# Performance work log

Measured on AMD Instinct MI355X. Metric: run time of the kernel, lower is better.

Reference implementation:

```python
import jax, jax.numpy as jnp
import numpy as np

N = 100_000   # nodes
E = 1_600_000 # edges
D = 64        # in = hidden = out channels
EPS = 1e-8


def setup_inputs() -> dict:
    key = jax.random.key(0)
    ks = jax.random.split(key, 6)
    s = 1.0 / np.sqrt(D)
    return {
        "x": jax.random.normal(ks[0], (N, D), jnp.float32),
        "edge_index": jax.random.randint(ks[1], (2, E), 0, N, dtype=jnp.int32),
        "W0": jax.random.normal(ks[2], (D, D), jnp.float32) * s,
        "b0": jnp.zeros((D,), jnp.float32),
        "Wm": jax.random.normal(ks[3], (D, D), jnp.float32) * s,
        "bm": jnp.zeros((D,), jnp.float32),
        "W1": jax.random.normal(ks[4], (D, D), jnp.float32) * s,
        "b1": jnp.zeros((D,), jnp.float32),
    }


def _proj_normalize(y):
    # projective (hyperbolic) renormalization onto the unit sphere in R^D
    return y / (jnp.linalg.norm(y, axis=-1, keepdims=True) + EPS)


def _hyp_linear(x, W, b):
    return _proj_normalize(x @ W + b)


def _hinner(u, v):
    # UHG (hyperbolic) bilinear form: <u,v> = u_1..d-1 . v_1..d-1 - u_d * v_d
    return jnp.sum(u[..., :-1] * v[..., :-1], axis=-1) - u[..., -1] * v[..., -1]


def _cross_ratio(x):
    a, b, c, d = x[0], x[1], x[2], x[3]
    return (_hinner(a, c) * _hinner(b, d)) / (_hinner(a, d) * _hinner(b, c) + EPS)


def _maybe_restore_cr(x, cr_init):
    # restore_cross_ratio: rescale x so the 4-point cross-ratio matches cr_init,
    # applied only when the torch guard conditions hold (finite, non-degenerate).
    cr_cur = _cross_ratio(x[:4])
    ratio = cr_init / (cr_cur + EPS)
    cond = ((~jnp.isnan(cr_cur)) & (~jnp.isnan(cr_init))
            & (jnp.abs(cr_cur) > EPS) & (jnp.abs(cr_init) > EPS)
            & (ratio > EPS))
    scale = jnp.where(cond, jnp.sqrt(jnp.abs(ratio)), 1.0)
    x_r = x * scale
    ok = jnp.all(jnp.isfinite(x_r))
    return jnp.where(cond & ok, x_r, x)


def _message_passing(x, src, dst, Wm, bm):
    # gather -> mean-aggregate(scatter) -> hyperbolic linear, preserving cross-ratio
    cr0 = _cross_ratio(x[:4])
    msgs = x[src]                                                  # [E, D] gather
    summed = jax.ops.segment_sum(msgs, dst, num_segments=N)        # [N, D] scatter-add
    cnt = jax.ops.segment_sum(jnp.ones((E,), x.dtype), dst, num_segments=N)
    agg = summed / jnp.maximum(cnt, 1.0)[:, None]                  # mean aggregation
    h = _proj_normalize(agg @ Wm + bm)
    return _maybe_restore_cr(h, cr0)


def reference(x, edge_index, W0, b0, Wm, bm, W1, b1):
    src, dst = edge_index[0], edge_index[1]
    cr_init = _cross_ratio(x[:4])          # N > 3 so has_cr is always True
    h = _hyp_linear(x, W0, b0)             # layers[0]
    # num_layers = 2 -> single message-passing round (i = 1)
    h = _message_passing(h, src, dst, Wm, bm)
    h = _hyp_linear(h, W1, b1)             # layers[1]
    h = jax.nn.relu(h)                      # act
    h = _maybe_restore_cr(h, cr_init)
    return h
```

## Files before the change

kernel.cpp:

```cpp
#include <hip/hip_runtime.h>
#include <math.h>

#define NNODES 100000
#define NEDGES 1600000
#define DD 64
#define EPS 1e-8f

#define NBUCK 1024
#define BW 98
#define BIN_BLOCKS 256
#define BIN_CHUNK ((NEDGES + BIN_BLOCKS - 1) / BIN_BLOCKS)
#define BIN_CAP 16
#define SORT_CAP 4096
#define NTILES (NNODES / 16)
#define CAP4 512
#define TSTR 68

typedef unsigned short us8 __attribute__((ext_vector_type(8)));
typedef short short8 __attribute__((ext_vector_type(8)));
typedef float f32x4 __attribute__((ext_vector_type(4)));

__device__ __forceinline__ float wave_sum(float v) {
    #pragma unroll
    for (int off = 32; off; off >>= 1) v += __shfl_xor(v, off, 64);
    return v;
}

__device__ __forceinline__ float hinner(float u, float v, float sgn) {
    return wave_sum(sgn * u * v);
}

__device__ __forceinline__ float cross_ratio(float r0, float r1, float r2, float r3, float sgn) {
    float A = hinner(r0, r2, sgn);
    float B = hinner(r1, r3, sgn);
    float C = hinner(r0, r3, sgn);
    float Dv = hinner(r1, r2, sgn);
    return (A * B) / (C * Dv + EPS);
}

__device__ __forceinline__ float restore_scale(float cr_i, float cr_c) {
    float ratio = cr_i / (cr_c + EPS);
    bool cond = (!__builtin_isnan(cr_c)) && (!__builtin_isnan(cr_i)) &&
                (fabsf(cr_c) > EPS) && (fabsf(cr_i) > EPS) && (ratio > EPS);
    float s = 1.0f;
    if (cond) {
        s = sqrtf(fabsf(ratio));
        if (!__builtin_isfinite(s)) s = 1.0f;
    }
    return s;
}

__device__ __forceinline__ unsigned short f2bf(float f) {
    unsigned u = __float_as_uint(f);
    unsigned r = (u + 0x7fffu + ((u >> 16) & 1u)) >> 16;
    return (unsigned short)r;
}

__device__ __forceinline__ float bf2f(unsigned short b) {
    return __uint_as_float(((unsigned)b) << 16);
}

__device__ __forceinline__ float bcast(float v, int lane) {
    return __int_as_float(__builtin_amdgcn_readlane(__float_as_int(v), lane));
}

__device__ __forceinline__ void load_bfrags(const float* __restrict__ W, int lane,
                                            short8 bhi[4][2], short8 blo[4][2]) {
    int c = lane & 15, q = lane >> 4;
    #pragma unroll
    for (int t = 0; t < 4; t++)
        #pragma unroll
        for (int h = 0; h < 2; h++) {
            short8 hi8, lo8;
            #pragma unroll
            for (int j = 0; j < 8; j++) {
                float w = W[(h * 32 + q * 8 + j) * DD + t * 16 + c];
                unsigned short hb = f2bf(w);
                float r = w - bf2f(hb);
                hi8[j] = (short)hb;
                lo8[j] = (short)f2bf(r);
            }
            bhi[t][h] = hi8;
            blo[t][h] = lo8;
        }
}

__device__ __forceinline__ void build_a8(const float av[8], short8& hi, short8& lo) {
    short8 h8, l8;
    #pragma unroll
    for (int j = 0; j < 8; j++) {
        unsigned short hb = f2bf(av[j]);
        float r = av[j] - bf2f(hb);
        h8[j] = (short)hb;
        l8[j] = (short)f2bf(r);
    }
    hi = h8;
    lo = l8;
}

__device__ __forceinline__ void build_a(const float* p, short8& hi, short8& lo) {
    float4 f0 = *(const float4*)p;
    float4 f1 = *(const float4*)(p + 4);
    float av[8] = {f0.x, f0.y, f0.z, f0.w, f1.x, f1.y, f1.z, f1.w};
    build_a8(av, hi, lo);
}

#define MFMA3R(cacc, ahi, alo, BH, BL, t, h)                                     \
    cacc = __builtin_amdgcn_mfma_f32_16x16x32_bf16(ahi, BH[t][h], cacc, 0, 0, 0); \
    cacc = __builtin_amdgcn_mfma_f32_16x16x32_bf16(alo, BH[t][h], cacc, 0, 0, 0); \
    cacc = __builtin_amdgcn_mfma_f32_16x16x32_bf16(ahi, BL[t][h], cacc, 0, 0, 0);

__global__ __launch_bounds__(256, 3) void k_l0h(const float* __restrict__ x,
                                                const float* __restrict__ W0,
                                                const float* __restrict__ b0,
                                                unsigned short* __restrict__ h0b,
                                                const int* __restrict__ ei,
                                                int* __restrict__ bhist) {
    __shared__ int h[NBUCK];
    if (blockIdx.x < 512) {
        for (int i = threadIdx.x; i < NBUCK; i += 256) h[i] = 0;
        __syncthreads();
        int tid = blockIdx.x * 256 + threadIdx.x;
        int stride = 512 * 256;
        for (int e = tid; e < NEDGES; e += stride)
            atomicAdd(&h[(unsigned)ei[NEDGES + e] / BW], 1);
        __syncthreads();
        for (int i = threadIdx.x; i < NBUCK; i += 256)
            if (h[i]) atomicAdd(&bhist[i], h[i]);
        return;
    }
    int bid = blockIdx.x - 512;
    int lane = threadIdx.x & 63;
    int c = lane & 15, q = lane >> 4;
    short8 bhi[4][2], blo[4][2];
    load_bfrags(W0, lane, bhi, blo);
    float badd[4];
    #pragma unroll
    for (int t = 0; t < 4; t++) badd[t] = b0[t * 16 + c];
    int wid = (bid * 256 + threadIdx.x) >> 6;
    int nw = (1024 * 256) >> 6;
    for (int tile = wid; tile < NTILES; tile += nw) {
        int R = tile * 16;
        f32x4 cc[4] = {{0, 0, 0, 0}, {0, 0, 0, 0}, {0, 0, 0, 0}, {0, 0, 0, 0}};
        #pragma unroll
        for (int hh = 0; hh < 2; hh++) {
            short8 ahi, alo;
            build_a(x + ((size_t)(R + c) << 6) + hh * 32 + q * 8, ahi, alo);
            #pragma unroll
            for (int t = 0; t < 4; t++) { MFMA3R(cc[t], ahi, alo, bhi, blo, t, hh); }
        }
        float ss[4];
        #pragma unroll
        for (int r = 0; r < 4; r++) {
            #pragma unroll
            for (int t = 0; t < 4; t++) cc[t][r] += badd[t];
            ss[r] = cc[0][r] * cc[0][r] + cc[1][r] * cc[1][r] +
                    cc[2][r] * cc[2][r] + cc[3][r] * cc[3][r];
        }
        #pragma unroll
        for (int off = 1; off <= 8; off <<= 1) {
            #pragma unroll
            for (int r = 0; r < 4; r++) ss[r] += __shfl_xor(ss[r], off, 64);
        }
        #pragma unroll
        for (int r = 0; r < 4; r++) {
            float sc = 1.0f / (sqrtf(ss[r]) + EPS);
            int row = R + q * 4 + r;
            #pragma unroll
            for (int t = 0; t < 4; t++)
                h0b[(size_t)row * DD + t * 16 + c] = f2bf(cc[t][r] * sc);
        }
    }
}

__global__ __launch_bounds__(NBUCK) void k_scan1024(const int* __restrict__ bhist,
                                                    int* __restrict__ bstart,
                                                    int* __restrict__ gcur,
                                                    int* __restrict__ scratch_cur) {
    __shared__ int s[NBUCK];
    int t = threadIdx.x;
    int v = bhist[t];
    s[t] = v;
    __syncthreads();
    for (int off = 1; off < NBUCK; off <<= 1) {
        int u = (t >= off) ? s[t - off] : 0;
        __syncthreads();
        s[t] += u;
        __syncthreads();
    }
    bstart[t] = s[t] - v;
    gcur[t] = s[t] - v;
    if (t == 0) scratch_cur[0] = 0;
}

__global__ __launch_bounds__(256) void k_bin(const int* __restrict__ ei,
                                             int* __restrict__ gcur,
                                             unsigned* __restrict__ colpack,
                                             int* __restrict__ cnt4,
                                             int* __restrict__ list4) {
    __shared__ unsigned stag[NBUCK * BIN_CAP];
    __shared__ int lcnt[NBUCK];
    int t = threadIdx.x;
    for (int i = t; i < NBUCK; i += 256) lcnt[i] = 0;
    __syncthreads();
    int lo = blockIdx.x * BIN_CHUNK;
    int hi = lo + BIN_CHUNK; if (hi > NEDGES) hi = NEDGES;
    for (int e = lo + t; e < hi; e += 256) {
        int d = ei[NEDGES + e];
        int s = ei[e];
        if ((unsigned)d < 4u) {
            int p = atomicAdd(&cnt4[d], 1);
            if (p < CAP4) list4[d * CAP4 + p] = s;
        }
        unsigned b = (unsigned)d / BW;
        unsigned dl = (unsigned)d - b * BW;
        unsigned pk = ((unsigned)s << 8) | dl;
        int slot = atomicAdd(&lcnt[b], 1);
        if (slot < BIN_CAP) {
            stag[b * BIN_CAP + slot] = pk;
        } else {
            colpack[atomicAdd(&gcur[b], 1)] = pk;
        }
    }
    __syncthreads();
    for (int b = t; b < NBUCK; b += 256) {
        int cnt = lcnt[b];
        if (cnt > BIN_CAP) cnt = BIN_CAP;
        if (cnt > 0) {
            int base = atomicAdd(&gcur[b], cnt);
            for (int i = 0; i < cnt; i++)
                colpack[base + i] = stag[b * BIN_CAP + i];
        }
    }
}

__global__ __launch_bounds__(512, 4) void k_sortAggH(const unsigned* __restrict__ colpack,
                                                     const int* __restrict__ bstart,
                                                     const int* __restrict__ bhist,
                                                     const unsigned short* __restrict__ h0b,
                                                     float* __restrict__ agg,
                                                     int* __restrict__ scratch,
                                                     int* __restrict__ scratch_cur,
                                                     const float* __restrict__ x,
                                                     const float* __restrict__ W0,
                                                     const float* __restrict__ b0,
                                                     const int* __restrict__ cnt4,
                                                     const int* __restrict__ list4,
                                                     const float* __restrict__ Wm,
                                                     const float* __restrict__ bm,
                                                     const float* __restrict__ W1,
                                                     const float* __restrict__ b1,
                                                     float* __restrict__ scal) {
    __shared__ int lcol[SORT_CAP];
    __shared__ int cnt[BW];
    __shared__ int pre[BW];
    __shared__ int sbs;
    int t = threadIdx.x;
    if (blockIdx.x == 0) {
        float* hs  = (float*)lcol;
        float* h2s = hs + 4 * DD;
        float* frs = h2s + 4 * DD;
        int lane = t & 63;
        int w = t >> 6;
        float sgn = (lane == 63) ? -1.0f : 1.0f;
        float s1 = 1.0f;
        float cr_init = 0.0f;
        if (w < 4) {
            float w0[DD];
            #pragma unroll
            for (int k = 0; k < DD; k++) w0[k] = W0[k * DD + lane];
            float b0v = b0[lane];
            auto h0row = [&](int r) -> float {
                float xv = x[(size_t)r * DD + lane];
                float acc = b0v;
                #pragma unroll
                for (int k = 0; k < DD; k++)
                    acc = fmaf(bcast(xv, k), w0[k], acc);
                float n = sqrtf(wave_sum(acc * acc));
                return acc / (n + EPS);
            };
            hs[w * DD + lane] = h0row(w);
            int full = cnt4[w];
            int cl = full; if (cl > CAP4) cl = CAP4;
            float sum = 0.0f;
            for (int i = 0; i < cl; i++) sum += h0row(list4[w * CAP4 + i]);
            float av = sum / fmaxf((float)full, 1.0f);
            float acc = bm[lane];
            #pragma unroll
            for (int k = 0; k < DD; k++)
                acc = fmaf(bcast(av, k), Wm[k * DD + lane], acc);
            float n = sqrtf(wave_sum(acc * acc));
            h2s[w * DD + lane] = acc / (n + EPS);
        }
        __syncthreads();
        if (w < 4) {
            cr_init = cross_ratio(x[lane], x[DD + lane], x[2 * DD + lane], x[3 * DD + lane], sgn);
            float cr0 = cross_ratio(hs[lane], hs[DD + lane], hs[2 * DD + lane], hs[3 * DD + lane], sgn);
            float cr_cur = cross_ratio(h2s[lane], h2s[DD + lane], h2s[2 * DD + lane], h2s[3 * DD + lane], sgn);
            s1 = restore_scale(cr0, cr_cur);
            float hv = h2s[w * DD + lane] * s1;
            float acc2 = b1[lane];
            #pragma unroll
            for (int k = 0; k < DD; k++)
                acc2 = fmaf(bcast(hv, k), W1[k * DD + lane], acc2);
            float n = sqrtf(wave_sum(acc2 * acc2));
            frs[w * DD + lane] = fmaxf(acc2 / (n + EPS), 0.0f);
        }
        __syncthreads();
        if (w == 0) {
            float cr2 = cross_ratio(frs[lane], frs[DD + lane], frs[2 * DD + lane], frs[3 * DD + lane], sgn);
            float s2 = restore_scale(cr_init, cr2);
            if (lane == 0) { scal[0] = s1; scal[1] = s2; }
        }
        return;
    }
    int b = blockIdx.x - 1;
    int nlo = b * BW; if (nlo > NNODES) nlo = NNODES;
    int nhi = nlo + BW; if (nhi > NNODES) nhi = NNODES;
    int nodes = nhi - nlo;
    int base = bstart[b];
    int n = bhist[b];
    for (int i = t; i < BW; i += 512) cnt[i] = 0;
    bool inLds = (n <= SORT_CAP);
    if (t == 0) sbs = inLds ? 0 : atomicAdd(scratch_cur, n);
    __syncthreads();
    int sb = sbs;
    for (int i = t; i < n; i += 512)
        atomicAdd(&cnt[colpack[base + i] & 255u], 1);
    __syncthreads();
    if (t < 64) {
        int v0 = cnt[t];
        int inc0 = v0;
        #pragma unroll
        for (int off = 1; off < 64; off <<= 1) {
            int u = __shfl_up(inc0, off, 64);
            if (t >= off) inc0 += u;
        }
        int tot0 = __builtin_amdgcn_readlane(inc0, 63);
        int ex0 = inc0 - v0;
        int i1 = 64 + t;
        int v1 = (i1 < BW) ? cnt[i1] : 0;
        int inc1 = v1;
        #pragma unroll
        for (int off = 1; off < 64; off <<= 1) {
            int u = __shfl_up(inc1, off, 64);
            if (t >= off) inc1 += u;
        }
        int ex1 = inc1 - v1 + tot0;
        pre[t] = ex0;
        cnt[t] = ex0;
        if (i1 < BW) { pre[i1] = ex1; cnt[i1] = ex1; }
    }
    __syncthreads();
    for (int i = t; i < n; i += 512) {
        unsigned pk = colpack[base + i];
        int pos = atomicAdd(&cnt[pk & 255u], 1);
        int v = (int)(pk >> 8);
        if (inLds) lcol[pos] = v;
        else       scratch[sb + pos] = v;
    }
    __syncthreads();
    int wv = t >> 6, lane = t & 63;
    int q = lane & 7, g = lane >> 3;
    auto run_agg = [&](auto ld) {
        for (int dl = wv; dl < nodes; dl += 8) {
            int start = pre[dl];
            int end = cnt[dl];
            float s[8] = {0, 0, 0, 0, 0, 0, 0, 0};
            int j0 = start;
            for (; j0 + 16 <= end; j0 += 16) {
                int s0 = ld(j0 + g);
                int s1i = ld(j0 + 8 + g);
                us8 u0 = *(const us8*)(h0b + (size_t)s0 * DD + q * 8);
                us8 u1 = *(const us8*)(h0b + (size_t)s1i * DD + q * 8);
                #pragma unroll
                for (int i = 0; i < 8; i++)
                    s[i] += bf2f(u0[i]) + bf2f(u1[i]);
            }
            for (; j0 < end; j0 += 8) {
                int e = j0 + g;
                bool val = e < end;
                int src = 0;
                if (val) src = ld(e);
                us8 u = *(const us8*)(h0b + (size_t)src * DD + q * 8);
                float f = val ? 1.0f : 0.0f;
                #pragma unroll
                for (int i = 0; i < 8; i++)
                    s[i] = fmaf(f, bf2f(u[i]), s[i]);
            }
            #pragma unroll
            for (int i = 0; i < 8; i++) {
                s[i] += __shfl_xor(s[i], 8, 64);
                s[i] += __shfl_xor(s[i], 16, 64);
                s[i] += __shfl_xor(s[i], 32, 64);
            }
            if (g == 0) {
                float inv = 1.0f / fmaxf((float)(end - start), 1.0f);
                float4* dst = (float4*)(agg + (size_t)(nlo + dl) * DD + q * 8);
                float4 o0 = {s[0] * inv, s[1] * inv, s[2] * inv, s[3] * inv};
                float4 o1 = {s[4] * inv, s[5] * inv, s[6] * inv, s[7] * inv};
                dst[0] = o0;
                dst[1] = o1;
            }
        }
    };
    if (inLds) run_agg([&](int e) { return lcol[e]; });
    else       run_agg([&](int e) { return scratch[sb + e]; });
}

__global__ __launch_bounds__(256, 2) void k_gemm2(float* data,
                                                  const float* __restrict__ Wm,
                                                  const float* __restrict__ bm,
                                                  const float* __restrict__ W1,
                                                  const float* __restrict__ b1,
                                                  const float* __restrict__ scal) {
    __shared__ float tsm[4][16 * TSTR];
    int tid = threadIdx.x;
    int wv = tid >> 6, lane = tid & 63;
    int c = lane & 15, q = lane >> 4;
    short8 bhiM[4][2], bloM[4][2], bhi1[4][2], blo1[4][2];
    load_bfrags(Wm, lane, bhiM, bloM);
    load_bfrags(W1, lane, bhi1, blo1);
    float bmv[4], b1v[4];
    #pragma unroll
    for (int t = 0; t < 4; t++) { bmv[t] = bm[t * 16 + c]; b1v[t] = b1[t * 16 + c]; }
    float s1 = scal[0], s2 = scal[1];
    int wid = (blockIdx.x * 256 + tid) >> 6;
    int nw = (gridDim.x * 256) >> 6;
    for (int tile = wid; tile < NTILES; tile += nw) {
        int R = tile * 16;
        f32x4 cc[4] = {{0, 0, 0, 0}, {0, 0, 0, 0}, {0, 0, 0, 0}, {0, 0, 0, 0}};
        #pragma unroll
        for (int hh = 0; hh < 2; hh++) {
            short8 ahi, alo;
            build_a(data + ((size_t)(R + c) << 6) + hh * 32 + q * 8, ahi, alo);
            #pragma unroll
            for (int t = 0; t < 4; t++) { MFMA3R(cc[t], ahi, alo, bhiM, bloM, t, hh); }
        }
        float ss[4];
        #pragma unroll
        for (int r = 0; r < 4; r++) {
            #pragma unroll
            for (int t = 0; t < 4; t++) cc[t][r] += bmv[t];
            ss[r] = cc[0][r] * cc[0][r] + cc[1][r] * cc[1][r] +
                    cc[2][r] * cc[2][r] + cc[3][r] * cc[3][r];
        }
        #pragma unroll
        for (int off = 1; off <= 8; off <<= 1) {
            #pragma unroll
            for (int r = 0; r < 4; r++) ss[r] += __shfl_xor(ss[r], off, 64);
        }
        #pragma unroll
        for (int r = 0; r < 4; r++) {
            float sc = s1 / (sqrtf(ss[r]) + EPS);
            #pragma unroll
            for (int t = 0; t < 4; t++)
                tsm[wv][(q * 4 + r) * TSTR + t * 16 + c] = cc[t][r] * sc;
        }
        f32x4 c2[4] = {{0, 0, 0, 0}, {0, 0, 0, 0}, {0, 0, 0, 0}, {0, 0, 0, 0}};
        #pragma unroll
        for (int hh = 0; hh < 2; hh++) {
            const float* p = &tsm[wv][c * TSTR + hh * 32 + q * 8];
            float av[8];
            #pragma unroll
            for (int j = 0; j < 8; j++) av[j] = p[j];
            short8 ahi, alo;
            build_a8(av, ahi, alo);
            #pragma unroll
            for (int t = 0; t < 4; t++) { MFMA3R(c2[t], ahi, alo, bhi1, blo1, t, hh); }
        }
        #pragma unroll
        for (int r = 0; r < 4; r++) {
            #pragma unroll
            for (int t = 0; t < 4; t++) c2[t][r] += b1v[t];
            ss[r] = c2[0][r] * c2[0][r] + c2[1][r] * c2[1][r] +
                    c2[2][r] * c2[2][r] + c2[3][r] * c2[3][r];
        }
        #pragma unroll
        for (int off = 1; off <= 8; off <<= 1) {
            #pragma unroll
            for (int r = 0; r < 4; r++) ss[r] += __shfl_xor(ss[r], off, 64);
        }
        #pragma unroll
        for (int r = 0; r < 4; r++) {
            float sc = 1.0f / (sqrtf(ss[r]) + EPS);
            int row = R + q * 4 + r;
            #pragma unroll
            for (int t = 0; t < 4; t++)
                data[(size_t)row * DD + t * 16 + c] = fmaxf(c2[t][r] * sc, 0.0f) * s2;
        }
    }
}

extern "C" void kernel_launch(void* const* d_in, const int* in_sizes, int n_in,
                              void* d_out, int out_size, void* d_ws, size_t ws_size,
                              hipStream_t stream) {
    const float* x  = (const float*)d_in[0];
    const int*   ei = (const int*)d_in[1];
    const float* W0 = (const float*)d_in[2];
    const float* b0 = (const float*)d_in[3];
    const float* Wm = (const float*)d_in[4];
    const float* bm = (const float*)d_in[5];
    const float* W1 = (const float*)d_in[6];
    const float* b1 = (const float*)d_in[7];
    float* out = (float*)d_out;

    unsigned short* h0b = (unsigned short*)d_ws;
    int* scratch = (int*)(h0b + (size_t)NNODES * DD);
    unsigned* colpack = (unsigned*)(scratch + NNODES);
    int* bhist  = (int*)(colpack + NEDGES);
    int* cnt4   = bhist + NBUCK;
    int* bstart = cnt4 + 4;
    int* gcur   = bstart + NBUCK;
    int* scur   = gcur + NBUCK;
    int* list4  = scur + 1;
    float* scal = (float*)(list4 + 4 * CAP4);

    (void)hipMemsetAsync(bhist, 0, (NBUCK + 4) * sizeof(int), stream);

    k_l0h     <<<1536, 256, 0, stream>>>(x, W0, b0, h0b, ei, bhist);
    k_scan1024<<<1, NBUCK, 0, stream>>>(bhist, bstart, gcur, scur);
    k_bin     <<<BIN_BLOCKS, 256, 0, stream>>>(ei, gcur, colpack, cnt4, list4);
    k_sortAggH<<<NBUCK, 512, 0, stream>>>(colpack, bstart, bhist, h0b, out, scratch, scur,
                                          x, W0, b0, cnt4, list4, Wm, bm, W1, b1, scal);
    k_gemm2   <<<512, 256, 0, stream>>>(out, Wm, bm, W1, b1, scal);
}
```

Before: 215.7 us.

## Assign one node per 8-lane group in aggregation instead of one node per wave

The gather/mean-aggregation loop now gives each 8-lane group its own destination node, so a wave handles 8 nodes at once rather than splitting one node's edges across its 8 groups. This removes the three cross-group shuffle reductions per node, and each group walks its node's edges four at a time with predicated loads. Iterations are padded to the largest degree among the wave's 8 nodes, which adds masked work for imbalanced degrees. The launch-bounds occupancy hint is also raised from 4 to 6, which may limit registers per thread.

```diff
diff --git a/kernel.cpp b/kernel.cpp
--- a/kernel.cpp
+++ b/kernel.cpp
@@ -234,7 +234,7 @@
     }
 }
 
-__global__ __launch_bounds__(512, 4) void k_sortAggH(const unsigned* __restrict__ colpack,
+__global__ __launch_bounds__(512, 6) void k_sortAggH(const unsigned* __restrict__ colpack,
                                                      const int* __restrict__ bstart,
                                                      const int* __restrict__ bhist,
                                                      const unsigned short* __restrict__ h0b,
@@ -362,40 +362,53 @@
     __syncthreads();
     int wv = t >> 6, lane = t & 63;
     int q = lane & 7, g = lane >> 3;
+    int S = wv * 8 + g;
     auto run_agg = [&](auto ld) {
-        for (int dl = wv; dl < nodes; dl += 8) {
-            int start = pre[dl];
-            int end = cnt[dl];
+        for (int b0 = 0; b0 < nodes; b0 += 64) {
+            int dl = b0 + S;
+            bool nv = dl < nodes;
+            int start = nv ? pre[dl] : 0;
+            int end   = nv ? cnt[dl] : 0;
+            int deg = end - start;
+            int md = deg, m1;
+            m1 = __shfl_xor(md, 8, 64);  md = md > m1 ? md : m1;
+            m1 = __shfl_xor(md, 16, 64); md = md > m1 ? md : m1;
+            m1 = __shfl_xor(md, 32, 64); md = md > m1 ? md : m1;
             float s[8] = {0, 0, 0, 0, 0, 0, 0, 0};
-            int j0 = start;
-            for (; j0 + 16 <= end; j0 += 16) {
-                int s0 = ld(j0 + g);
-                int s1i = ld(j0 + 8 + g);
+            int j = 0;
+            for (; j + 4 <= md; j += 4) {
+                int e0 = (j + 0 < deg) ? start + j + 0 : 0;
+                int e1 = (j + 1 < deg) ? start + j + 1 : 0;
+                int e2 = (j + 2 < deg) ? start + j + 2 : 0;
+                int e3 = (j + 3 < deg) ? start + j + 3 : 0;
+                int s0 = ld(e0), s1i = ld(e1), s2i = ld(e2), s3i = ld(e3);
+                us8 u0 = *(const us8*)(h0b + (size_t)s0  * DD + q * 8);
+                us8 u1 = *(const us8*)(h0b + (size_t)s1i * DD + q * 8);
+                us8 u2 = *(const us8*)(h0b + (size_t)s2i * DD + q * 8);
+                us8 u3 = *(const us8*)(h0b + (size_t)s3i * DD + q * 8);
+                float f0 = (j + 0 < deg) ? 1.0f : 0.0f;
+                float f1 = (j + 1 < deg) ? 1.0f : 0.0f;
+                float f2 = (j + 2 < deg) ? 1.0f : 0.0f;
+                float f3 = (j + 3 < deg) ? 1.0f : 0.0f;
+                #pragma unroll
+                for (int i = 0; i < 8; i++) {
+                    s[i] = fmaf(f0, bf2f(u0[i]), s[i]);
+                    s[i] = fmaf(f1, bf2f(u1[i]), s[i]);
+                    s[i] = fmaf(f2, bf2f(u2[i]), s[i]);
+                    s[i] = fmaf(f3, bf2f(u3[i]), s[i]);
+                }
+            }
+            for (; j < md; j++) {
+                int e0 = (j < deg) ? start + j : 0;
+                int s0 = ld(e0);
                 us8 u0 = *(const us8*)(h0b + (size_t)s0 * DD + q * 8);
-                us8 u1 = *(const us8*)(h0b + (size_t)s1i * DD + q * 8);
+                float f0 = (j < deg) ? 1.0f : 0.0f;
                 #pragma unroll
                 for (int i = 0; i < 8; i++)
-                    s[i] += bf2f(u0[i]) + bf2f(u1[i]);
+                    s[i] = fmaf(f0, bf2f(u0[i]), s[i]);
             }
-            for (; j0 < end; j0 += 8) {
-                int e = j0 + g;
-                bool val = e < end;
-                int src = 0;
-                if (val) src = ld(e);
-                us8 u = *(const us8*)(h0b + (size_t)src * DD + q * 8);
-                float f = val ? 1.0f : 0.0f;
-                #pragma unroll
-                for (int i = 0; i < 8; i++)
-                    s[i] = fmaf(f, bf2f(u[i]), s[i]);
-            }
-            #pragma unroll
-            for (int i = 0; i < 8; i++) {
-                s[i] += __shfl_xor(s[i], 8, 64);
-                s[i] += __shfl_xor(s[i], 16, 64);
-                s[i] += __shfl_xor(s[i], 32, 64);
-            }
-            if (g == 0) {
-                float inv = 1.0f / fmaxf((float)(end - start), 1.0f);
+            if (nv) {
+                float inv = 1.0f / fmaxf((float)deg, 1.0f);
                 float4* dst = (float4*)(agg + (size_t)(nlo + dl) * DD + q * 8);
                 float4 o0 = {s[0] * inv, s[1] * inv, s[2] * inv, s[3] * inv};
                 float4 o1 = {s[4] * inv, s[5] * inv, s[6] * inv, s[7] * inv};
```

After: 223.3 us. 3.5% more time.

## Fold bucket scan into histogram kernel and precompute per-node degrees

Applied to the files above, without the earlier changes.

The histogram blocks of the first kernel now also count per-node in-degree with global atomics. The last histogram block to finish, found through an atomic counter, runs the 1024-bucket exclusive scan, so the separate scan kernel launch goes away. The sort/aggregate kernel seeds its per-node counts from the precomputed degrees, skipping its LDS-atomic counting pass over colpack. In exchange it adds 1.6M random global atomics and an extra 400KB memset. The degree array aliases the overflow scratch buffer, which could be corrupted if any bucket spills out of LDS.

```diff
diff --git a/kernel.cpp b/kernel.cpp
--- a/kernel.cpp
+++ b/kernel.cpp
@@ -115,18 +115,60 @@
                                                 const float* __restrict__ b0,
                                                 unsigned short* __restrict__ h0b,
                                                 const int* __restrict__ ei,
-                                                int* __restrict__ bhist) {
+                                                int* __restrict__ bhist,
+                                                int* __restrict__ deg,
+                                                int* __restrict__ lbctr,
+                                                int* __restrict__ bstart,
+                                                int* __restrict__ gcur,
+                                                int* __restrict__ scur) {
     __shared__ int h[NBUCK];
+    __shared__ int wtot[4];
+    __shared__ int lastf;
     if (blockIdx.x < 512) {
         for (int i = threadIdx.x; i < NBUCK; i += 256) h[i] = 0;
         __syncthreads();
         int tid = blockIdx.x * 256 + threadIdx.x;
         int stride = 512 * 256;
-        for (int e = tid; e < NEDGES; e += stride)
-            atomicAdd(&h[(unsigned)ei[NEDGES + e] / BW], 1);
+        for (int e = tid; e < NEDGES; e += stride) {
+            int d = ei[NEDGES + e];
+            atomicAdd(&h[(unsigned)d / BW], 1);
+            atomicAdd(&deg[d], 1);
+        }
         __syncthreads();
         for (int i = threadIdx.x; i < NBUCK; i += 256)
             if (h[i]) atomicAdd(&bhist[i], h[i]);
+        __threadfence();
+        if (threadIdx.x == 0) lastf = (atomicAdd(lbctr, 1) == 511);
+        __syncthreads();
+        if (!lastf) return;
+        __threadfence();
+        int t = threadIdx.x;
+        int v[4];
+        int s = 0;
+        #pragma unroll
+        for (int k = 0; k < 4; k++) {
+            v[k] = atomicAdd(&bhist[t * 4 + k], 0);
+            s += v[k];
+        }
+        int lane = t & 63, w = t >> 6;
+        int inc = s;
+        #pragma unroll
+        for (int off = 1; off < 64; off <<= 1) {
+            int u = __shfl_up(inc, off, 64);
+            if (lane >= off) inc += u;
+        }
+        if (lane == 63) wtot[w] = inc;
+        __syncthreads();
+        int wbase = 0;
+        for (int i = 0; i < w; i++) wbase += wtot[i];
+        int run = wbase + inc - s;
+        #pragma unroll
+        for (int k = 0; k < 4; k++) {
+            bstart[t * 4 + k] = run;
+            gcur[t * 4 + k] = run;
+            run += v[k];
+        }
+        if (t == 0) scur[0] = 0;
         return;
     }
     int bid = blockIdx.x - 512;
@@ -171,26 +213,6 @@
                 h0b[(size_t)row * DD + t * 16 + c] = f2bf(cc[t][r] * sc);
         }
     }
-}
-
-__global__ __launch_bounds__(NBUCK) void k_scan1024(const int* __restrict__ bhist,
-                                                    int* __restrict__ bstart,
-                                                    int* __restrict__ gcur,
-                                                    int* __restrict__ scratch_cur) {
-    __shared__ int s[NBUCK];
-    int t = threadIdx.x;
-    int v = bhist[t];
-    s[t] = v;
-    __syncthreads();
-    for (int off = 1; off < NBUCK; off <<= 1) {
-        int u = (t >= off) ? s[t - off] : 0;
-        __syncthreads();
-        s[t] += u;
-        __syncthreads();
-    }
-    bstart[t] = s[t] - v;
-    gcur[t] = s[t] - v;
-    if (t == 0) scratch_cur[0] = 0;
 }
 
 __global__ __launch_bounds__(256) void k_bin(const int* __restrict__ ei,
@@ -237,6 +259,7 @@
 __global__ __launch_bounds__(512, 4) void k_sortAggH(const unsigned* __restrict__ colpack,
                                                      const int* __restrict__ bstart,
                                                      const int* __restrict__ bhist,
+                                                     const int* __restrict__ deg,
                                                      const unsigned short* __restrict__ h0b,
                                                      float* __restrict__ agg,
                                                      int* __restrict__ scratch,
@@ -320,14 +343,11 @@
     int nodes = nhi - nlo;
     int base = bstart[b];
     int n = bhist[b];
-    for (int i = t; i < BW; i += 512) cnt[i] = 0;
+    for (int i = t; i < BW; i += 512) cnt[i] = (nlo + i < nhi) ? deg[nlo + i] : 0;
     bool inLds = (n <= SORT_CAP);
     if (t == 0) sbs = inLds ? 0 : atomicAdd(scratch_cur, n);
     __syncthreads();
     int sb = sbs;
-    for (int i = t; i < n; i += 512)
-        atomicAdd(&cnt[colpack[base + i] & 255u], 1);
-    __syncthreads();
     if (t < 64) {
         int v0 = cnt[t];
         int inc0 = v0;
@@ -507,21 +527,23 @@
 
     unsigned short* h0b = (unsigned short*)d_ws;
     int* scratch = (int*)(h0b + (size_t)NNODES * DD);
+    int* deg = scratch;
     unsigned* colpack = (unsigned*)(scratch + NNODES);
     int* bhist  = (int*)(colpack + NEDGES);
     int* cnt4   = bhist + NBUCK;
-    int* bstart = cnt4 + 4;
+    int* lbctr  = cnt4 + 4;
+    int* bstart = lbctr + 1;
     int* gcur   = bstart + NBUCK;
     int* scur   = gcur + NBUCK;
     int* list4  = scur + 1;
     float* scal = (float*)(list4 + 4 * CAP4);
 
-    (void)hipMemsetAsync(bhist, 0, (NBUCK + 4) * sizeof(int), stream);
-
-    k_l0h     <<<1536, 256, 0, stream>>>(x, W0, b0, h0b, ei, bhist);
-    k_scan1024<<<1, NBUCK, 0, stream>>>(bhist, bstart, gcur, scur);
+    (void)hipMemsetAsync(deg, 0, NNODES * sizeof(int), stream);
+    (void)hipMemsetAsync(bhist, 0, (NBUCK + 5) * sizeof(int), stream);
+
+    k_l0h     <<<1536, 256, 0, stream>>>(x, W0, b0, h0b, ei, bhist, deg, lbctr, bstart, gcur, scur);
     k_bin     <<<BIN_BLOCKS, 256, 0, stream>>>(ei, gcur, colpack, cnt4, list4);
-    k_sortAggH<<<NBUCK, 512, 0, stream>>>(colpack, bstart, bhist, h0b, out, scratch, scur,
+    k_sortAggH<<<NBUCK, 512, 0, stream>>>(colpack, bstart, bhist, deg, h0b, out, scratch, scur,
                                           x, W0, b0, cnt4, list4, Wm, bm, W1, b1, scal);
     k_gemm2   <<<512, 256, 0, stream>>>(out, Wm, bm, W1, b1, scal);
 }
```

Result: slower. 314.2 us (+45.6%).

## Replace per-bucket counting sort with LDS float atomic accumulation

Applied to the files above, without the earlier changes.

Drops the in-block counting sort of each bucket's edges by destination. Each wave instead takes a contiguous slice of the bucket's edges, gathers the bf16 source rows and adds them into a per-bucket LDS accumulator with float atomics, counting degrees the same way. The aim is to remove the histogram, scan and scatter passes and the global scratch fallback. In exchange it issues many LDS float atomics per edge, which can contend and makes the summation order nondeterministic.

```diff
diff --git a/kernel.cpp b/kernel.cpp
--- a/kernel.cpp
+++ b/kernel.cpp
@@ -11,10 +11,10 @@
 #define BIN_BLOCKS 256
 #define BIN_CHUNK ((NEDGES + BIN_BLOCKS - 1) / BIN_BLOCKS)
 #define BIN_CAP 16
-#define SORT_CAP 4096
 #define NTILES (NNODES / 16)
 #define CAP4 512
 #define TSTR 68
+#define ASTR 65
 
 typedef unsigned short us8 __attribute__((ext_vector_type(8)));
 typedef short short8 __attribute__((ext_vector_type(8)));
@@ -234,30 +234,26 @@
     }
 }
 
-__global__ __launch_bounds__(512, 4) void k_sortAggH(const unsigned* __restrict__ colpack,
-                                                     const int* __restrict__ bstart,
-                                                     const int* __restrict__ bhist,
-                                                     const unsigned short* __restrict__ h0b,
-                                                     float* __restrict__ agg,
-                                                     int* __restrict__ scratch,
-                                                     int* __restrict__ scratch_cur,
-                                                     const float* __restrict__ x,
-                                                     const float* __restrict__ W0,
-                                                     const float* __restrict__ b0,
-                                                     const int* __restrict__ cnt4,
-                                                     const int* __restrict__ list4,
-                                                     const float* __restrict__ Wm,
-                                                     const float* __restrict__ bm,
-                                                     const float* __restrict__ W1,
-                                                     const float* __restrict__ b1,
-                                                     float* __restrict__ scal) {
-    __shared__ int lcol[SORT_CAP];
-    __shared__ int cnt[BW];
-    __shared__ int pre[BW];
-    __shared__ int sbs;
+__global__ __launch_bounds__(512, 4) void k_aggH(const unsigned* __restrict__ colpack,
+                                                 const int* __restrict__ bstart,
+                                                 const int* __restrict__ bhist,
+                                                 const unsigned short* __restrict__ h0b,
+                                                 float* __restrict__ agg,
+                                                 const float* __restrict__ x,
+                                                 const float* __restrict__ W0,
+                                                 const float* __restrict__ b0,
+                                                 const int* __restrict__ cnt4,
+                                                 const int* __restrict__ list4,
+                                                 const float* __restrict__ Wm,
+                                                 const float* __restrict__ bm,
+                                                 const float* __restrict__ W1,
+                                                 const float* __restrict__ b1,
+                                                 float* __restrict__ scal) {
+    __shared__ float acc[BW][ASTR];
+    __shared__ int dcnt[BW];
     int t = threadIdx.x;
     if (blockIdx.x == 0) {
-        float* hs  = (float*)lcol;
+        float* hs  = &acc[0][0];
         float* h2s = hs + 4 * DD;
         float* frs = h2s + 4 * DD;
         int lane = t & 63;
@@ -272,12 +268,12 @@
             float b0v = b0[lane];
             auto h0row = [&](int r) -> float {
                 float xv = x[(size_t)r * DD + lane];
-                float acc = b0v;
+                float acc2 = b0v;
                 #pragma unroll
                 for (int k = 0; k < DD; k++)
-                    acc = fmaf(bcast(xv, k), w0[k], acc);
-                float n = sqrtf(wave_sum(acc * acc));
-                return acc / (n + EPS);
+                    acc2 = fmaf(bcast(xv, k), w0[k], acc2);
+                float n = sqrtf(wave_sum(acc2 * acc2));
+                return acc2 / (n + EPS);
             };
             hs[w * DD + lane] = h0row(w);
             int full = cnt4[w];
@@ -285,12 +281,12 @@
             float sum = 0.0f;
             for (int i = 0; i < cl; i++) sum += h0row(list4[w * CAP4 + i]);
             float av = sum / fmaxf((float)full, 1.0f);
-            float acc = bm[lane];
+            float acc2 = bm[lane];
             #pragma unroll
             for (int k = 0; k < DD; k++)
-                acc = fmaf(bcast(av, k), Wm[k * DD + lane], acc);
-            float n = sqrtf(wave_sum(acc * acc));
-            h2s[w * DD + lane] = acc / (n + EPS);
+                acc2 = fmaf(bcast(av, k), Wm[k * DD + lane], acc2);
+            float n = sqrtf(wave_sum(acc2 * acc2));
+            h2s[w * DD + lane] = acc2 / (n + EPS);
         }
         __syncthreads();
         if (w < 4) {
@@ -315,97 +311,62 @@
         return;
     }
     int b = blockIdx.x - 1;
-    int nlo = b * BW; if (nlo > NNODES) nlo = NNODES;
+    int nlo = b * BW;
+    if (nlo >= NNODES) return;
     int nhi = nlo + BW; if (nhi > NNODES) nhi = NNODES;
     int nodes = nhi - nlo;
     int base = bstart[b];
     int n = bhist[b];
-    for (int i = t; i < BW; i += 512) cnt[i] = 0;
-    bool inLds = (n <= SORT_CAP);
-    if (t == 0) sbs = inLds ? 0 : atomicAdd(scratch_cur, n);
-    __syncthreads();
-    int sb = sbs;
-    for (int i = t; i < n; i += 512)
-        atomicAdd(&cnt[colpack[base + i] & 255u], 1);
-    __syncthreads();
-    if (t < 64) {
-        int v0 = cnt[t];
-        int inc0 = v0;
-        #pragma unroll
-        for (int off = 1; off < 64; off <<= 1) {
-            int u = __shfl_up(inc0, off, 64);
-            if (t >= off) inc0 += u;
-        }
-        int tot0 = __builtin_amdgcn_readlane(inc0, 63);
-        int ex0 = inc0 - v0;
-        int i1 = 64 + t;
-        int v1 = (i1 < BW) ? cnt[i1] : 0;
-        int inc1 = v1;
-        #pragma unroll
-        for (int off = 1; off < 64; off <<= 1) {
-            int u = __shfl_up(inc1, off, 64);
-            if (t >= off) inc1 += u;
-        }
-        int ex1 = inc1 - v1 + tot0;
-        pre[t] = ex0;
-        cnt[t] = ex0;
-        if (i1 < BW) { pre[i1] = ex1; cnt[i1] = ex1; }
-    }
-    __syncthreads();
-    for (int i = t; i < n; i += 512) {
-        unsigned pk = colpack[base + i];
-        int pos = atomicAdd(&cnt[pk & 255u], 1);
-        int v = (int)(pk >> 8);
-        if (inLds) lcol[pos] = v;
-        else       scratch[sb + pos] = v;
-    }
+    for (int i = t; i < BW * ASTR; i += 512) (&acc[0][0])[i] = 0.0f;
+    for (int i = t; i < BW; i += 512) dcnt[i] = 0;
     __syncthreads();
     int wv = t >> 6, lane = t & 63;
     int q = lane & 7, g = lane >> 3;
-    auto run_agg = [&](auto ld) {
-        for (int dl = wv; dl < nodes; dl += 8) {
-            int start = pre[dl];
-            int end = cnt[dl];
-            float s[8] = {0, 0, 0, 0, 0, 0, 0, 0};
-            int j0 = start;
-            for (; j0 + 16 <= end; j0 += 16) {
-                int s0 = ld(j0 + g);
-                int s1i = ld(j0 + 8 + g);
-                us8 u0 = *(const us8*)(h0b + (size_t)s0 * DD + q * 8);
-                us8 u1 = *(const us8*)(h0b + (size_t)s1i * DD + q * 8);
+    int chunk = (n + 7) >> 3;
+    int wlo = wv * chunk;
+    int whi = wlo + chunk; if (whi > n) whi = n;
+    if (whi > wlo) {
+        int last = whi - 1;
+        for (int jb = wlo; jb < whi; jb += 32) {
+            unsigned pkv[4];
+            float mm[4];
+            #pragma unroll
+            for (int u = 0; u < 4; u++) {
+                int j = jb + u * 8 + g;
+                int jc = j < last ? j : last;
+                pkv[u] = colpack[base + jc];
+                mm[u] = (j < whi) ? 1.0f : 0.0f;
+            }
+            us8 vv[4];
+            #pragma unroll
+            for (int u = 0; u < 4; u++)
+                vv[u] = *(const us8*)(h0b + (size_t)(pkv[u] >> 8) * DD + q * 8);
+            #pragma unroll
+            for (int u = 0; u < 4; u++) {
+                int dl = pkv[u] & 255u;
+                float* a = &acc[dl][q * 8];
                 #pragma unroll
                 for (int i = 0; i < 8; i++)
-                    s[i] += bf2f(u0[i]) + bf2f(u1[i]);
+                    atomicAdd(&a[i], mm[u] * bf2f(vv[u][i]));
+                if (q == 0 && mm[u] != 0.0f) atomicAdd(&dcnt[dl], 1);
             }
-            for (; j0 < end; j0 += 8) {
-                int e = j0 + g;
-                bool val = e < end;
-                int src = 0;
-                if (val) src = ld(e);
-                us8 u = *(const us8*)(h0b + (size_t)src * DD + q * 8);
-                float f = val ? 1.0f : 0.0f;
-                #pragma unroll
-                for (int i = 0; i < 8; i++)
-                    s[i] = fmaf(f, bf2f(u[i]), s[i]);
+        }
+    }
+    __syncthreads();
+    if (t < BW * 4) {
+        int dl = t >> 2;
+        if (dl < nodes) {
+            int c0 = (t & 3) * 16;
+            float inv = 1.0f / fmaxf((float)dcnt[dl], 1.0f);
+            float4* dst = (float4*)(agg + (size_t)(nlo + dl) * DD + c0);
+            #pragma unroll
+            for (int k4 = 0; k4 < 4; k4++) {
+                float4 o = {acc[dl][c0 + k4 * 4 + 0] * inv, acc[dl][c0 + k4 * 4 + 1] * inv,
+                            acc[dl][c0 + k4 * 4 + 2] * inv, acc[dl][c0 + k4 * 4 + 3] * inv};
+                dst[k4] = o;
             }
-            #pragma unroll
-            for (int i = 0; i < 8; i++) {
-                s[i] += __shfl_xor(s[i], 8, 64);
-                s[i] += __shfl_xor(s[i], 16, 64);
-                s[i] += __shfl_xor(s[i], 32, 64);
-            }
-            if (g == 0) {
-                float inv = 1.0f / fmaxf((float)(end - start), 1.0f);
-                float4* dst = (float4*)(agg + (size_t)(nlo + dl) * DD + q * 8);
-                float4 o0 = {s[0] * inv, s[1] * inv, s[2] * inv, s[3] * inv};
-                float4 o1 = {s[4] * inv, s[5] * inv, s[6] * inv, s[7] * inv};
-                dst[0] = o0;
-                dst[1] = o1;
-            }
-        }
-    };
-    if (inLds) run_agg([&](int e) { return lcol[e]; });
-    else       run_agg([&](int e) { return scratch[sb + e]; });
+        }
+    }
 }
 
 __global__ __launch_bounds__(256, 2) void k_gemm2(float* data,
@@ -521,7 +482,7 @@
     k_l0h     <<<1536, 256, 0, stream>>>(x, W0, b0, h0b, ei, bhist);
     k_scan1024<<<1, NBUCK, 0, stream>>>(bhist, bstart, gcur, scur);
     k_bin     <<<BIN_BLOCKS, 256, 0, stream>>>(ei, gcur, colpack, cnt4, list4);
-    k_sortAggH<<<NBUCK, 512, 0, stream>>>(colpack, bstart, bhist, h0b, out, scratch, scur,
+    k_aggH    <<<NBUCK, 512, 0, stream>>>(colpack, bstart, bhist, h0b, out,
                                           x, W0, b0, cnt4, list4, Wm, bm, W1, b1, scal);
     k_gemm2   <<<512, 256, 0, stream>>>(out, Wm, bm, W1, b1, scal);
 }
```

New measurement: 757.4 us. 251% more time.
